# Optimization experiments

Measured on AMD Instinct MI355X. Metric: run time of the kernel, lower is better.

Reference implementation:

```python
import jax, jax.numpy as jnp
import numpy as np

B, N, C = 16, 256, 512
H, E = 8, 64
HD = C // H
SCALE = HD ** -0.5


def setup_inputs() -> dict:
    key = jax.random.key(0)
    ks = jax.random.split(key, 10)
    s = 0.02
    return {
        "node_embeds": jax.random.normal(ks[0], (B, N, C), jnp.float32),
        "edge_embeds": jax.random.normal(ks[1], (B, E, N, N), jnp.float32),
        "padding_mask": jnp.zeros((B, 1, N, N), bool),
        # params (torch Linear: y = x @ W.T + b, W is [out,in]; 1x1 Conv2d -> [out,in])
        "qkv_w": jax.random.normal(ks[2], (3 * C, C), jnp.float32) * s,
        "proj_w": jax.random.normal(ks[3], (C, C), jnp.float32) * s,
        "proj_b": jnp.zeros((C,), jnp.float32),
        "reduce_w": jax.random.normal(ks[4], (H, E), jnp.float32) * s,
        "reduce_b": jnp.zeros((H,), jnp.float32),
        "expand_w": jax.random.normal(ks[5], (E, H), jnp.float32) * s,
        "expand_b": jnp.zeros((E,), jnp.float32),
        "fc_w": jax.random.normal(ks[6], (C, E), jnp.float32) * s,
        "fc_b": jnp.zeros((C,), jnp.float32),
    }


def reference(node_embeds, edge_embeds, padding_mask, qkv_w, proj_w, proj_b,
              reduce_w, reduce_b, expand_w, expand_b, fc_w, fc_b):
    # qkv projection -> q,k,v each [B,H,N,HD]
    qkv = (node_embeds @ qkv_w.T).reshape(B, N, 3, H, HD)
    qkv = jnp.transpose(qkv, (2, 0, 3, 1, 4))
    q, k, v = qkv[0], qkv[1], qkv[2]

    attn = jnp.einsum("bhnd,bhmd->bhnm", q, k) * SCALE  # [B,H,N,N]
    # reduce: 1x1 conv over edge channels -> per-head bias
    attn_bias = jnp.einsum("bexy,he->bhxy", edge_embeds, reduce_w) + reduce_b[None, :, None, None]
    attn = attn + attn_bias
    residual = attn

    attn_sm = jax.nn.softmax(jnp.where(padding_mask, -jnp.inf, attn), axis=-1)
    node_out = jnp.einsum("bhnm,bhmd->bnhd", attn_sm, v).reshape(B, N, C)

    # expand: 1x1 conv heads -> edge channels on (attn_sm + residual)
    edge_out = jnp.einsum("bhxy,eh->bexy", attn_sm + residual, expand_w) + expand_b[None, :, None, None]

    # edge-update pooling: masked softmax over last dim, weighted sum
    w = jax.nn.softmax(jnp.where(padding_mask, -jnp.inf, edge_out), axis=-1)
    w = jnp.einsum("bexy->bxe", (w * edge_out).sum(-1)[:, :, :, None].squeeze(-1)[:, :, :, None].squeeze(-1)[..., None].squeeze(-1)[:, None].squeeze(1).reshape(B, E, N).transpose(0, 2, 1) * 1.0) if False else jnp.transpose((w * edge_out).sum(-1), (0, 2, 1))  # [B,N,E]

    node_out = node_out + (w @ fc_w.T + fc_b)
    node_out = node_out @ proj_w.T + proj_b
    return node_out, edge_out
```

## Files before the change

kernel.cpp:

```cpp
#include <hip/hip_runtime.h>
#include <hip/hip_bf16.h>
#include <cstdint>
#include <cstddef>

#define SCALE_ 0.125f

typedef float f4_ __attribute__((ext_vector_type(4)));
typedef __bf16 bf2_ __attribute__((ext_vector_type(2)));
typedef short bf8f_ __attribute__((ext_vector_type(8)));
typedef float f32x4_ __attribute__((ext_vector_type(4)));

__device__ __forceinline__ unsigned pk2(float a, float b) {
  union { __hip_bfloat16 h[2]; unsigned u; } x;
  x.h[0] = __float2bfloat16(a);
  x.h[1] = __float2bfloat16(b);
  return x.u;
}
__device__ __forceinline__ unsigned short bf16b(float a) {
  union { __hip_bfloat16 h; unsigned short s; } x;
  x.h = __float2bfloat16(a);
  return x.s;
}
__device__ __forceinline__ float blo(unsigned u) { return __uint_as_float(u << 16); }
__device__ __forceinline__ float bhi(unsigned u) { return __uint_as_float(u & 0xffff0000u); }
__device__ __forceinline__ float b2f(unsigned short s) { return __uint_as_float(((unsigned)s) << 16); }

__device__ __forceinline__ float dot2b(unsigned a, unsigned b, float c) {
#if __has_builtin(__builtin_amdgcn_fdot2_f32_bf16)
  return __builtin_amdgcn_fdot2_f32_bf16(__builtin_bit_cast(bf2_, a),
                                         __builtin_bit_cast(bf2_, b), c, false);
#else
  return fmaf(blo(a), blo(b), fmaf(bhi(a), bhi(b), c));
#endif
}

template<int CTRL, int RM>
__device__ __forceinline__ float dppadd(float v) {
  int x = __builtin_amdgcn_update_dpp(0, __float_as_int(v), CTRL, RM, 0xf, true);
  return v + __int_as_float(x);
}
__device__ __forceinline__ float wave_sum64(float v) {
  v = dppadd<0x111, 0xf>(v);
  v = dppadd<0x112, 0xf>(v);
  v = dppadd<0x114, 0xf>(v);
  v = dppadd<0x118, 0xf>(v);
  v = dppadd<0x142, 0xa>(v);
  v = dppadd<0x143, 0xc>(v);
  return __int_as_float(__builtin_amdgcn_readlane(__float_as_int(v), 63));
}

__global__ __launch_bounds__(256) void qkv_gemm(
    const float* __restrict__ X, const float* __restrict__ W,
    unsigned short* __restrict__ qb, uint2* __restrict__ ktq, uint2* __restrict__ vq)
{
  __shared__ alignas(16) unsigned ABbuf[128*36 + 64*36];
  unsigned* A_pk = ABbuf;
  unsigned* B_pk = ABbuf + 128*36;
  unsigned short* A16 = (unsigned short*)A_pk;
  unsigned short* B16 = (unsigned short*)B_pk;
  unsigned short* C16 = (unsigned short*)ABbuf;

  const int t  = threadIdx.x;
  const int lane = t & 63;
  const int wv = t >> 6;
  const int m0 = blockIdx.x * 128;
  const int o0 = blockIdx.y * 64;
  const int wrow = wv * 32;

  f32x4_ acc[2][4];
  #pragma unroll
  for (int fm = 0; fm < 2; fm++)
    #pragma unroll
    for (int fn = 0; fn < 4; fn++) acc[fm][fn] = (f32x4_){0.f, 0.f, 0.f, 0.f};

  const float4* X4 = (const float4*)X;
  const float4* W4 = (const float4*)W;

  for (int cc = 0; cc < 512; cc += 64) {
    #pragma unroll
    for (int i = 0; i < 8; i++) {
      int id = t + 256*i;
      int row = id >> 4, c4 = id & 15;
      float4 a = X4[(size_t)(m0 + row)*128 + (cc >> 2) + c4];
      A_pk[row*36 + c4*2    ] = pk2(a.x, a.y);
      A_pk[row*36 + c4*2 + 1] = pk2(a.z, a.w);
    }
    #pragma unroll
    for (int i = 0; i < 4; i++) {
      int id = t + 256*i;
      int row = id >> 4, c4 = id & 15;
      float4 w = W4[(size_t)(o0 + row)*128 + (cc >> 2) + c4];
      B_pk[row*36 + c4*2    ] = pk2(w.x, w.y);
      B_pk[row*36 + c4*2 + 1] = pk2(w.z, w.w);
    }
    __syncthreads();
    #pragma unroll
    for (int ks = 0; ks < 64; ks += 32) {
      const int kb = ks + (lane >> 4)*8;
      bf8f_ af0 = *(const bf8f_*)&A16[(wrow      + (lane & 15))*72 + kb];
      bf8f_ af1 = *(const bf8f_*)&A16[(wrow + 16 + (lane & 15))*72 + kb];
      #pragma unroll
      for (int fn = 0; fn < 4; fn++) {
        bf8f_ bf = *(const bf8f_*)&B16[(fn*16 + (lane & 15))*72 + kb];
        acc[0][fn] = __builtin_amdgcn_mfma_f32_16x16x32_bf16(af0, bf, acc[0][fn], 0, 0, 0);
        acc[1][fn] = __builtin_amdgcn_mfma_f32_16x16x32_bf16(af1, bf, acc[1][fn], 0, 0, 0);
      }
    }
    __syncthreads();
  }

  #pragma unroll
  for (int fm = 0; fm < 2; fm++)
    #pragma unroll
    for (int fn = 0; fn < 4; fn++)
      #pragma unroll
      for (int r = 0; r < 4; r++)
        C16[(wrow + fm*16 + (lane >> 4)*4 + r)*68 + fn*16 + (lane & 15)] =
          bf16b(acc[fm][fn][r]);
  __syncthreads();

  const int tm = (t & 15) * 8;
  const int to = (t >> 4) * 4;
  const int three = o0 >> 9;
  const int h = (o0 >> 6) & 7;
  if (three == 0) {
    #pragma unroll
    for (int i = 0; i < 8; i++) {
      int m = m0 + tm + i;
      int b = m >> 8, n = m & 255;
      uint2 u = *(const uint2*)&C16[(tm + i)*68 + to];
      *(uint2*)&qb[((size_t)(b*8 + h)*256 + n)*64 + to] = u;
    }
  } else if (three == 1) {
    #pragma unroll
    for (int i = 0; i < 8; i++) {
      int m = m0 + tm + i;
      int b = m >> 8, n = m & 255;
      uint2 u = *(const uint2*)&C16[(tm + i)*68 + to];
      ktq[(size_t)(b*8 + h)*4096 + (size_t)(to >> 2)*256 + n] = u;
    }
  } else {
    int m = m0 + tm;
    int b = m >> 8, n0 = m & 255;
    #pragma unroll
    for (int ii = 0; ii < 2; ii++) {
      #pragma unroll
      for (int j = 0; j < 4; j++) {
        unsigned ua = C16[(tm + 4*ii    )*68 + to + j];
        unsigned ub = C16[(tm + 4*ii + 1)*68 + to + j];
        unsigned uc = C16[(tm + 4*ii + 2)*68 + to + j];
        unsigned ud = C16[(tm + 4*ii + 3)*68 + to + j];
        vq[(size_t)(b*8 + h)*4096 + (size_t)((n0 >> 2) + ii)*64 + to + j] =
          make_uint2(ua | (ub << 16), uc | (ud << 16));
      }
    }
  }
}

__global__ __launch_bounds__(256) void fused_attn(
    const unsigned short* __restrict__ qb, const uint2* __restrict__ ktq,
    const uint2* __restrict__ vq,
    const float* __restrict__ edge, const unsigned char* __restrict__ mask,
    const float* __restrict__ rw, const float* __restrict__ rb,
    const float* __restrict__ ew, const float* __restrict__ eb,
    const float* __restrict__ fcw, const float* __restrict__ fcb,
    float* __restrict__ out_edge, unsigned short* __restrict__ tmpb)
{
  __shared__ alignas(16) unsigned q_pk[4][8][32];
  __shared__ alignas(16) unsigned char pt_raw[16896];
  __shared__ alignas(16) unsigned short nacc16[4][512];
  __shared__ alignas(16) unsigned rw_pk[32][8];
  __shared__ alignas(16) unsigned ew_pk[64][4];
  __shared__ alignas(16) float eb_s[64];
  __shared__ alignas(16) float pl2[4][64];
  __shared__ alignas(16) float inv_s[4][8];

  unsigned short (*p_sb)[8][264] = (unsigned short (*)[8][264])pt_raw;
  unsigned (*t8_pk)[4][264] = (unsigned (*)[4][264])pt_raw;

  const int t = threadIdx.x;
  const int lane = t & 63;
  const int wv = t >> 6;
  const int b = blockIdx.x >> 6;
  const int x0 = (blockIdx.x & 63) * 4;
  const int y = t;

  #pragma unroll
  for (int i = 0; i < 4; i++) {
    int id = t + i*256;
    int r = id >> 8, rest = id & 255;
    int h = rest >> 5, d2 = rest & 31;
    q_pk[r][h][d2] =
      *(const unsigned*)&qb[((size_t)(b*8 + h)*256 + x0 + r)*64 + d2*2];
  }
  { int epx = t >> 3, h = t & 7;
    rw_pk[epx][h] = pk2(rw[h*64 + 2*epx], rw[h*64 + 2*epx + 1]); }
  { int e = t >> 2, hp = t & 3;
    ew_pk[e][hp] = pk2(ew[(size_t)e*8 + 2*hp], ew[(size_t)e*8 + 2*hp + 1]); }
  if (t < 64) eb_s[t] = eb[t];
  float madd[4];
  #pragma unroll
  for (int r = 0; r < 4; r++)
    madd[r] = mask[(size_t)b*65536 + (size_t)(x0 + r)*256 + y] ? -1e30f : 0.f;
  __syncthreads();

  float acc[4][8];
  #pragma unroll
  for (int h = 0; h < 8; h++) {
    float rv = rb[h];
    #pragma unroll
    for (int r = 0; r < 4; r++) acc[r][h] = rv;
  }
  {
    const float* ep = edge + (size_t)b*(64*65536) + (size_t)x0*256 + y;
    #pragma unroll
    for (int h = 0; h < 8; h++) {
      const uint2* kq = ktq + (size_t)(b*8 + h)*4096 + y;
      float qk[4] = {0.f, 0.f, 0.f, 0.f};
      #pragma unroll
      for (int i = 0; i < 4; i++) {
        const int e2 = h*4 + i;
        unsigned vp[4];
        #pragma unroll
        for (int r = 0; r < 4; r++) {
          float a = __builtin_nontemporal_load(ep + (size_t)(2*e2)*65536 + r*256);
          float c = __builtin_nontemporal_load(ep + (size_t)(2*e2+1)*65536 + r*256);
          vp[r] = pk2(a, c);
        }
        uint4 w0 = *(const uint4*)&rw_pk[e2][0];
        uint4 w1 = *(const uint4*)&rw_pk[e2][4];
        unsigned wh[8] = {w0.x,w0.y,w0.z,w0.w,w1.x,w1.y,w1.z,w1.w};
        #pragma unroll
        for (int r = 0; r < 4; r++)
          #pragma unroll
          for (int hh = 0; hh < 8; hh++)
            acc[r][hh] = dot2b(vp[r], wh[hh], acc[r][hh]);
        #pragma unroll
        for (int dd = 0; dd < 4; dd++) {
          const int d4 = i*4 + dd;
          uint2 k = kq[(size_t)d4*256];
          #pragma unroll
          for (int r = 0; r < 4; r++) {
            uint2 qa = *(const uint2*)&q_pk[r][h][d4*2];
            qk[r] = dot2b(k.x, qa.x, qk[r]);
            qk[r] = dot2b(k.y, qa.y, qk[r]);
          }
        }
      }
      #pragma unroll
      for (int r = 0; r < 4; r++) acc[r][h] += SCALE_ * qk[r];
    }
  }

  #pragma unroll
  for (int r = 0; r < 4; r++)
    #pragma unroll
    for (int h = 0; h < 8; h++)
      p_sb[r][h][y] = bf16b(__expf(acc[r][h] + madd[r]));
  __syncthreads();

  {
    const int h = t >> 5;
    const int i2 = t & 31;
    const int d0 = i2 * 2;
    const unsigned ONES = 0x3F803F80u;
    const uint4* vp4 = (const uint4*)(vq + (size_t)(b*8 + h)*4096);
    float a[4][2], ps[4];
    #pragma unroll
    for (int r = 0; r < 4; r++) { a[r][0] = 0.f; a[r][1] = 0.f; ps[r] = 0.f; }
    #pragma unroll 2
    for (int y4 = 0; y4 < 64; y4++) {
      uint4 u = vp4[(size_t)y4*32 + i2];
      #pragma unroll
      for (int r = 0; r < 4; r++) {
        uint2 pp = *(const uint2*)&p_sb[r][h][y4*4];
        a[r][0] = dot2b(pp.x, u.x, a[r][0]); a[r][0] = dot2b(pp.y, u.y, a[r][0]);
        a[r][1] = dot2b(pp.x, u.z, a[r][1]); a[r][1] = dot2b(pp.y, u.w, a[r][1]);
        ps[r] = dot2b(pp.x, ONES, ps[r]);    ps[r] = dot2b(pp.y, ONES, ps[r]);
      }
    }
    #pragma unroll
    for (int r = 0; r < 4; r++) {
      float inv = 1.0f / ps[r];
      *(unsigned*)&nacc16[r][h*64 + d0] = pk2(a[r][0]*inv, a[r][1]*inv);
      if (i2 == 0) inv_s[r][h] = inv;
    }
  }
  __syncthreads();

  #pragma unroll
  for (int r = 0; r < 4; r++) {
    float v[8];
    #pragma unroll
    for (int h = 0; h < 8; h++)
      v[h] = __expf(acc[r][h] + madd[r]) * inv_s[r][h] + acc[r][h];
    t8_pk[r][0][y] = pk2(v[0], v[1]);
    t8_pk[r][1][y] = pk2(v[2], v[3]);
    t8_pk[r][2][y] = pk2(v[4], v[5]);
    t8_pk[r][3][y] = pk2(v[6], v[7]);
  }
  __syncthreads();

  {
    const int r = wv;
    const int y0 = lane * 4;
    const int xg = x0 + r;
    uint4 tfq[4];
    #pragma unroll
    for (int hp = 0; hp < 4; hp++) tfq[hp] = *(const uint4*)&t8_pk[r][hp][y0];
    uchar4 mb = *(const uchar4*)&mask[(size_t)b*65536 + (size_t)xg*256 + y0];
    const float md0 = mb.x ? -1e30f : 0.f;
    const float md1 = mb.y ? -1e30f : 0.f;
    const float md2 = mb.z ? -1e30f : 0.f;
    const float md3 = mb.w ? -1e30f : 0.f;
    for (int e = 0; e < 64; e++) {
      uint4 w = *(const uint4*)&ew_pk[e][0];
      float ebv = eb_s[e];
      float eo0 = dot2b(tfq[3].x, w.w, dot2b(tfq[2].x, w.z,
                  dot2b(tfq[1].x, w.y, dot2b(tfq[0].x, w.x, ebv))));
      float eo1 = dot2b(tfq[3].y, w.w, dot2b(tfq[2].y, w.z,
                  dot2b(tfq[1].y, w.y, dot2b(tfq[0].y, w.x, ebv))));
      float eo2 = dot2b(tfq[3].z, w.w, dot2b(tfq[2].z, w.z,
                  dot2b(tfq[1].z, w.y, dot2b(tfq[0].z, w.x, ebv))));
      float eo3 = dot2b(tfq[3].w, w.w, dot2b(tfq[2].w, w.z,
                  dot2b(tfq[1].w, w.y, dot2b(tfq[0].w, w.x, ebv))));
      float e0v = __expf(eo0+md0), e1v = __expf(eo1+md1);
      float e2v = __expf(eo2+md2), e3v = __expf(eo3+md3);
      float se  = (e0v + e1v) + (e2v + e3v);
      float swe = (e0v*eo0 + e1v*eo1) + (e2v*eo2 + e3v*eo3);
      se  = wave_sum64(se);
      swe = wave_sum64(swe);
      if (lane == 0) pl2[r][e] = swe / se;
      f4_ ov = {eo0, eo1, eo2, eo3};
      __builtin_nontemporal_store(ov,
        (f4_*)&out_edge[((size_t)(b*64 + e)*256 + xg)*256 + y0]);
    }
  }
  __syncthreads();

  #pragma unroll
  for (int pass = 0; pass < 2; pass++) {
    int cdx = t + pass*256;
    float bias_c = fcb[cdx];
    float a[4];
    #pragma unroll
    for (int r = 0; r < 4; r++) a[r] = b2f(nacc16[r][cdx]) + bias_c;
    const float4* fw4 = (const float4*)fcw;
    #pragma unroll 4
    for (int e4 = 0; e4 < 16; e4++) {
      float4 f = fw4[(size_t)cdx*16 + e4];
      #pragma unroll
      for (int r = 0; r < 4; r++) {
        float4 pl = *(const float4*)&pl2[r][e4*4];
        a[r] += pl.x*f.x + pl.y*f.y + pl.z*f.z + pl.w*f.w;
      }
    }
    #pragma unroll
    for (int r = 0; r < 4; r++)
      tmpb[((size_t)b*256 + x0 + r)*512 + cdx] = bf16b(a[r]);
  }
}

__global__ __launch_bounds__(256) void proj_gemm(
    const unsigned short* __restrict__ Xb, const float* __restrict__ W,
    const float* __restrict__ bias, float* __restrict__ out)
{
  __shared__ alignas(16) unsigned A_pk[8][132];
  __shared__ alignas(16) unsigned W_pk[8][68];
  const int t  = threadIdx.x;
  const int m0 = blockIdx.x * 128;
  const int o0 = blockIdx.y * 64;
  const int tm = (t & 15) * 8;
  const int to = (t >> 4) * 4;
  float acc[8][4];
  #pragma unroll
  for (int i = 0; i < 8; i++)
    #pragma unroll
    for (int j = 0; j < 4; j++) acc[i][j] = 0.f;

  const uint4* X4 = (const uint4*)Xb;
  const float4* W4 = (const float4*)W;
  for (int c0 = 0; c0 < 512; c0 += 16) {
    {
      int row = t >> 1, half = t & 1;
      uint4 a = X4[(size_t)(m0 + row) * 64 + (c0 >> 3) + half];
      A_pk[half*4 + 0][row] = a.x;
      A_pk[half*4 + 1][row] = a.y;
      A_pk[half*4 + 2][row] = a.z;
      A_pk[half*4 + 3][row] = a.w;
    }
    {
      int row = t >> 2, quad = t & 3;
      float4 w = W4[(size_t)(o0 + row) * 128 + (c0 >> 2) + quad];
      W_pk[quad*2    ][row] = pk2(w.x, w.y);
      W_pk[quad*2 + 1][row] = pk2(w.z, w.w);
    }
    __syncthreads();
    #pragma unroll
    for (int kp = 0; kp < 8; kp++) {
      uint4 a0 = *(const uint4*)&A_pk[kp][tm];
      uint4 a1 = *(const uint4*)&A_pk[kp][tm + 4];
      uint4 w0 = *(const uint4*)&W_pk[kp][to];
      unsigned am[8] = {a0.x,a0.y,a0.z,a0.w,a1.x,a1.y,a1.z,a1.w};
      unsigned wn[4] = {w0.x,w0.y,w0.z,w0.w};
      #pragma unroll
      for (int i = 0; i < 8; i++)
        #pragma unroll
        for (int j = 0; j < 4; j++) acc[i][j] = dot2b(am[i], wn[j], acc[i][j]);
    }
    __syncthreads();
  }
  float4 bb = *(const float4*)&bias[o0 + to];
  #pragma unroll
  for (int i = 0; i < 8; i++) {
    int m = m0 + tm + i;
    float4 r = make_float4(acc[i][0]+bb.x, acc[i][1]+bb.y, acc[i][2]+bb.z, acc[i][3]+bb.w);
    *(float4*)&out[(size_t)m*512 + o0 + to] = r;
  }
}

extern "C" void kernel_launch(void* const* d_in, const int* in_sizes, int n_in,
                              void* d_out, int out_size, void* d_ws, size_t ws_size,
                              hipStream_t stream)
{
  (void)in_sizes; (void)n_in; (void)out_size; (void)ws_size;
  const float* node   = (const float*)d_in[0];
  const float* edge   = (const float*)d_in[1];
  const unsigned char* mask = (const unsigned char*)d_in[2];
  const float* qkv_w  = (const float*)d_in[3];
  const float* proj_w = (const float*)d_in[4];
  const float* proj_b = (const float*)d_in[5];
  const float* rw     = (const float*)d_in[6];
  const float* rb     = (const float*)d_in[7];
  const float* ew     = (const float*)d_in[8];
  const float* eb     = (const float*)d_in[9];
  const float* fcw    = (const float*)d_in[10];
  const float* fcb    = (const float*)d_in[11];

  float* out_node = (float*)d_out;
  float* out_edge = out_node + (size_t)16*256*512;

  char* ws = (char*)d_ws;
  unsigned short* qb  = (unsigned short*)(ws);
  uint2*          ktq = (uint2*)         (ws + (size_t)4*1024*1024);
  uint2*          vq  = (uint2*)         (ws + (size_t)8*1024*1024);
  unsigned short* tmpb= (unsigned short*)(ws + (size_t)12*1024*1024);

  qkv_gemm <<<dim3(32, 24, 1), 256, 0, stream>>>(node, qkv_w, qb, ktq, vq);
  fused_attn<<<dim3(1024, 1, 1), 256, 0, stream>>>(qb, ktq, vq, edge, mask,
                                                   rw, rb, ew, eb, fcw, fcb,
                                                   out_edge, tmpb);
  proj_gemm<<<dim3(32, 8, 1), 256, 0, stream>>>(tmpb, proj_w, proj_b, out_node);
}
```

Before: 184.4 us.

## Use MFMA in projection GEMM and vectorize edge/key loads in fused attention

The projection GEMM drops its scalar dot2 bf16 loop in favour of MFMA 16x16x32 bf16 instructions, staging 64-wide K tiles in padded LDS. In the fused attention kernel, each thread now handles 2 rows x 2 adjacent columns instead of 4 rows x 1 column. This lets edge values load as float2 and K as uint4, and P is stored as packed bf16 pairs. The aim is fewer memory instructions and faster GEMM math, at the cost of changed LDS layouts and register use.

```diff
diff --git a/kernel.cpp b/kernel.cpp
--- a/kernel.cpp
+++ b/kernel.cpp
@@ -6,6 +6,7 @@
 #define SCALE_ 0.125f
 
 typedef float f4_ __attribute__((ext_vector_type(4)));
+typedef float f2_ __attribute__((ext_vector_type(2)));
 typedef __bf16 bf2_ __attribute__((ext_vector_type(2)));
 typedef short bf8f_ __attribute__((ext_vector_type(8)));
 typedef float f32x4_ __attribute__((ext_vector_type(4)));
@@ -175,7 +176,7 @@
   __shared__ alignas(16) float pl2[4][64];
   __shared__ alignas(16) float inv_s[4][8];
 
-  unsigned short (*p_sb)[8][264] = (unsigned short (*)[8][264])pt_raw;
+  unsigned (*p_pk)[8][132] = (unsigned (*)[8][132])pt_raw;
   unsigned (*t8_pk)[4][264] = (unsigned (*)[4][264])pt_raw;
 
   const int t = threadIdx.x;
@@ -183,7 +184,8 @@
   const int wv = t >> 6;
   const int b = blockIdx.x >> 6;
   const int x0 = (blockIdx.x & 63) * 4;
-  const int y = t;
+  const int yp = t & 127;
+  const int rg = t >> 7;
 
   #pragma unroll
   for (int i = 0; i < 4; i++) {
@@ -198,65 +200,80 @@
   { int e = t >> 2, hp = t & 3;
     ew_pk[e][hp] = pk2(ew[(size_t)e*8 + 2*hp], ew[(size_t)e*8 + 2*hp + 1]); }
   if (t < 64) eb_s[t] = eb[t];
-  float madd[4];
-  #pragma unroll
-  for (int r = 0; r < 4; r++)
-    madd[r] = mask[(size_t)b*65536 + (size_t)(x0 + r)*256 + y] ? -1e30f : 0.f;
-  __syncthreads();
-
-  float acc[4][8];
+  float madd[2][2];
+  #pragma unroll
+  for (int rr = 0; rr < 2; rr++) {
+    uchar2 mb = *(const uchar2*)&mask[(size_t)b*65536 + (size_t)(x0 + 2*rg + rr)*256 + 2*yp];
+    madd[rr][0] = mb.x ? -1e30f : 0.f;
+    madd[rr][1] = mb.y ? -1e30f : 0.f;
+  }
+  __syncthreads();
+
+  float acc[2][8][2];
   #pragma unroll
   for (int h = 0; h < 8; h++) {
     float rv = rb[h];
     #pragma unroll
-    for (int r = 0; r < 4; r++) acc[r][h] = rv;
+    for (int rr = 0; rr < 2; rr++) { acc[rr][h][0] = rv; acc[rr][h][1] = rv; }
   }
   {
-    const float* ep = edge + (size_t)b*(64*65536) + (size_t)x0*256 + y;
+    const float* ep = edge + (size_t)b*(64*65536) + (size_t)(x0 + 2*rg)*256 + 2*yp;
+    const uint4* kq4base = (const uint4*)(ktq + (size_t)(b*8)*4096);
     #pragma unroll
     for (int h = 0; h < 8; h++) {
-      const uint2* kq = ktq + (size_t)(b*8 + h)*4096 + y;
-      float qk[4] = {0.f, 0.f, 0.f, 0.f};
+      const uint4* kq4 = (const uint4*)(ktq + (size_t)(b*8 + h)*4096) ;
+      float qk[2][2] = {{0.f, 0.f}, {0.f, 0.f}};
       #pragma unroll
       for (int i = 0; i < 4; i++) {
         const int e2 = h*4 + i;
-        unsigned vp[4];
-        #pragma unroll
-        for (int r = 0; r < 4; r++) {
-          float a = __builtin_nontemporal_load(ep + (size_t)(2*e2)*65536 + r*256);
-          float c = __builtin_nontemporal_load(ep + (size_t)(2*e2+1)*65536 + r*256);
-          vp[r] = pk2(a, c);
-        }
+        f2_ A0 = __builtin_nontemporal_load((const f2_*)(ep + (size_t)(2*e2)*65536));
+        f2_ A1 = __builtin_nontemporal_load((const f2_*)(ep + (size_t)(2*e2)*65536 + 256));
+        f2_ B0 = __builtin_nontemporal_load((const f2_*)(ep + (size_t)(2*e2+1)*65536));
+        f2_ B1 = __builtin_nontemporal_load((const f2_*)(ep + (size_t)(2*e2+1)*65536 + 256));
+        unsigned vp00 = pk2(A0.x, B0.x);
+        unsigned vp01 = pk2(A0.y, B0.y);
+        unsigned vp10 = pk2(A1.x, B1.x);
+        unsigned vp11 = pk2(A1.y, B1.y);
         uint4 w0 = *(const uint4*)&rw_pk[e2][0];
         uint4 w1 = *(const uint4*)&rw_pk[e2][4];
         unsigned wh[8] = {w0.x,w0.y,w0.z,w0.w,w1.x,w1.y,w1.z,w1.w};
         #pragma unroll
-        for (int r = 0; r < 4; r++)
-          #pragma unroll
-          for (int hh = 0; hh < 8; hh++)
-            acc[r][hh] = dot2b(vp[r], wh[hh], acc[r][hh]);
+        for (int hh = 0; hh < 8; hh++) {
+          acc[0][hh][0] = dot2b(vp00, wh[hh], acc[0][hh][0]);
+          acc[0][hh][1] = dot2b(vp01, wh[hh], acc[0][hh][1]);
+          acc[1][hh][0] = dot2b(vp10, wh[hh], acc[1][hh][0]);
+          acc[1][hh][1] = dot2b(vp11, wh[hh], acc[1][hh][1]);
+        }
         #pragma unroll
         for (int dd = 0; dd < 4; dd++) {
           const int d4 = i*4 + dd;
-          uint2 k = kq[(size_t)d4*256];
+          uint4 kk = kq4[(size_t)d4*128 + yp];
           #pragma unroll
-          for (int r = 0; r < 4; r++) {
-            uint2 qa = *(const uint2*)&q_pk[r][h][d4*2];
-            qk[r] = dot2b(k.x, qa.x, qk[r]);
-            qk[r] = dot2b(k.y, qa.y, qk[r]);
+          for (int rr = 0; rr < 2; rr++) {
+            uint2 qa = *(const uint2*)&q_pk[2*rg + rr][h][d4*2];
+            qk[rr][0] = dot2b(kk.x, qa.x, qk[rr][0]);
+            qk[rr][0] = dot2b(kk.y, qa.y, qk[rr][0]);
+            qk[rr][1] = dot2b(kk.z, qa.x, qk[rr][1]);
+            qk[rr][1] = dot2b(kk.w, qa.y, qk[rr][1]);
           }
         }
       }
       #pragma unroll
-      for (int r = 0; r < 4; r++) acc[r][h] += SCALE_ * qk[r];
-    }
-  }
-
-  #pragma unroll
-  for (int r = 0; r < 4; r++)
+      for (int rr = 0; rr < 2; rr++) {
+        acc[rr][h][0] += SCALE_ * qk[rr][0];
+        acc[rr][h][1] += SCALE_ * qk[rr][1];
+      }
+    }
+    (void)kq4base;
+  }
+
+  #pragma unroll
+  for (int rr = 0; rr < 2; rr++)
     #pragma unroll
     for (int h = 0; h < 8; h++)
-      p_sb[r][h][y] = bf16b(__expf(acc[r][h] + madd[r]));
+      p_pk[2*rg + rr][h][yp] =
+        pk2(__expf(acc[rr][h][0] + madd[rr][0]),
+            __expf(acc[rr][h][1] + madd[rr][1]));
   __syncthreads();
 
   {
@@ -273,7 +290,7 @@
       uint4 u = vp4[(size_t)y4*32 + i2];
       #pragma unroll
       for (int r = 0; r < 4; r++) {
-        uint2 pp = *(const uint2*)&p_sb[r][h][y4*4];
+        uint2 pp = *(const uint2*)&p_pk[r][h][y4*2];
         a[r][0] = dot2b(pp.x, u.x, a[r][0]); a[r][0] = dot2b(pp.y, u.y, a[r][0]);
         a[r][1] = dot2b(pp.x, u.z, a[r][1]); a[r][1] = dot2b(pp.y, u.w, a[r][1]);
         ps[r] = dot2b(pp.x, ONES, ps[r]);    ps[r] = dot2b(pp.y, ONES, ps[r]);
@@ -289,15 +306,20 @@
   __syncthreads();
 
   #pragma unroll
-  for (int r = 0; r < 4; r++) {
-    float v[8];
-    #pragma unroll
-    for (int h = 0; h < 8; h++)
-      v[h] = __expf(acc[r][h] + madd[r]) * inv_s[r][h] + acc[r][h];
-    t8_pk[r][0][y] = pk2(v[0], v[1]);
-    t8_pk[r][1][y] = pk2(v[2], v[3]);
-    t8_pk[r][2][y] = pk2(v[4], v[5]);
-    t8_pk[r][3][y] = pk2(v[6], v[7]);
+  for (int rr = 0; rr < 2; rr++) {
+    const int r = 2*rg + rr;
+    #pragma unroll
+    for (int yy = 0; yy < 2; yy++) {
+      const int y = 2*yp + yy;
+      float v[8];
+      #pragma unroll
+      for (int h = 0; h < 8; h++)
+        v[h] = __expf(acc[rr][h][yy] + madd[rr][yy]) * inv_s[r][h] + acc[rr][h][yy];
+      t8_pk[r][0][y] = pk2(v[0], v[1]);
+      t8_pk[r][1][y] = pk2(v[2], v[3]);
+      t8_pk[r][2][y] = pk2(v[4], v[5]);
+      t8_pk[r][3][y] = pk2(v[6], v[7]);
+    }
   }
   __syncthreads();
 
@@ -365,57 +387,75 @@
     const unsigned short* __restrict__ Xb, const float* __restrict__ W,
     const float* __restrict__ bias, float* __restrict__ out)
 {
-  __shared__ alignas(16) unsigned A_pk[8][132];
-  __shared__ alignas(16) unsigned W_pk[8][68];
+  __shared__ alignas(16) unsigned ABbuf[128*36 + 64*36];
+  unsigned* A_pk = ABbuf;
+  unsigned* B_pk = ABbuf + 128*36;
+  unsigned short* A16 = (unsigned short*)A_pk;
+  unsigned short* B16 = (unsigned short*)B_pk;
+
   const int t  = threadIdx.x;
+  const int lane = t & 63;
+  const int wv = t >> 6;
   const int m0 = blockIdx.x * 128;
   const int o0 = blockIdx.y * 64;
-  const int tm = (t & 15) * 8;
-  const int to = (t >> 4) * 4;
-  float acc[8][4];
-  #pragma unroll
-  for (int i = 0; i < 8; i++)
-    #pragma unroll
-    for (int j = 0; j < 4; j++) acc[i][j] = 0.f;
+  const int wrow = wv * 32;
+
+  f32x4_ acc[2][4];
+  #pragma unroll
+  for (int fm = 0; fm < 2; fm++)
+    #pragma unroll
+    for (int fn = 0; fn < 4; fn++) acc[fm][fn] = (f32x4_){0.f, 0.f, 0.f, 0.f};
 
   const uint4* X4 = (const uint4*)Xb;
   const float4* W4 = (const float4*)W;
-  for (int c0 = 0; c0 < 512; c0 += 16) {
-    {
-      int row = t >> 1, half = t & 1;
-      uint4 a = X4[(size_t)(m0 + row) * 64 + (c0 >> 3) + half];
-      A_pk[half*4 + 0][row] = a.x;
-      A_pk[half*4 + 1][row] = a.y;
-      A_pk[half*4 + 2][row] = a.z;
-      A_pk[half*4 + 3][row] = a.w;
-    }
-    {
-      int row = t >> 2, quad = t & 3;
-      float4 w = W4[(size_t)(o0 + row) * 128 + (c0 >> 2) + quad];
-      W_pk[quad*2    ][row] = pk2(w.x, w.y);
-      W_pk[quad*2 + 1][row] = pk2(w.z, w.w);
+
+  for (int cc = 0; cc < 512; cc += 64) {
+    #pragma unroll
+    for (int i = 0; i < 4; i++) {
+      int id = t + 256*i;
+      int row = id >> 3, c8 = id & 7;
+      uint4 a = X4[(size_t)(m0 + row)*64 + (cc >> 3) + c8];
+      A_pk[row*36 + c8*4    ] = a.x;
+      A_pk[row*36 + c8*4 + 1] = a.y;
+      A_pk[row*36 + c8*4 + 2] = a.z;
+      A_pk[row*36 + c8*4 + 3] = a.w;
+    }
+    #pragma unroll
+    for (int i = 0; i < 4; i++) {
+      int id = t + 256*i;
+      int row = id >> 4, c4 = id & 15;
+      float4 w = W4[(size_t)(o0 + row)*128 + (cc >> 2) + c4];
+      B_pk[row*36 + c4*2    ] = pk2(w.x, w.y);
+      B_pk[row*36 + c4*2 + 1] = pk2(w.z, w.w);
     }
     __syncthreads();
     #pragma unroll
-    for (int kp = 0; kp < 8; kp++) {
-      uint4 a0 = *(const uint4*)&A_pk[kp][tm];
-      uint4 a1 = *(const uint4*)&A_pk[kp][tm + 4];
-      uint4 w0 = *(const uint4*)&W_pk[kp][to];
-      unsigned am[8] = {a0.x,a0.y,a0.z,a0.w,a1.x,a1.y,a1.z,a1.w};
-      unsigned wn[4] = {w0.x,w0.y,w0.z,w0.w};
-      #pragma unroll
-      for (int i = 0; i < 8; i++)
-        #pragma unroll
-        for (int j = 0; j < 4; j++) acc[i][j] = dot2b(am[i], wn[j], acc[i][j]);
+    for (int ks = 0; ks < 64; ks += 32) {
+      const int kb = ks + (lane >> 4)*8;
+      bf8f_ af0 = *(const bf8f_*)&A16[(wrow      + (lane & 15))*72 + kb];
+      bf8f_ af1 = *(const bf8f_*)&A16[(wrow + 16 + (lane & 15))*72 + kb];
+      #pragma unroll
+      for (int fn = 0; fn < 4; fn++) {
+        bf8f_ bf = *(const bf8f_*)&B16[(fn*16 + (lane & 15))*72 + kb];
+        acc[0][fn] = __builtin_amdgcn_mfma_f32_16x16x32_bf16(af0, bf, acc[0][fn], 0, 0, 0);
+        acc[1][fn] = __builtin_amdgcn_mfma_f32_16x16x32_bf16(af1, bf, acc[1][fn], 0, 0, 0);
+      }
     }
     __syncthreads();
   }
-  float4 bb = *(const float4*)&bias[o0 + to];
-  #pragma unroll
-  for (int i = 0; i < 8; i++) {
-    int m = m0 + tm + i;
-    float4 r = make_float4(acc[i][0]+bb.x, acc[i][1]+bb.y, acc[i][2]+bb.z, acc[i][3]+bb.w);
-    *(float4*)&out[(size_t)m*512 + o0 + to] = r;
+
+  #pragma unroll
+  for (int fn = 0; fn < 4; fn++) {
+    const int col = o0 + fn*16 + (lane & 15);
+    const float bb = bias[col];
+    #pragma unroll
+    for (int fm = 0; fm < 2; fm++) {
+      #pragma unroll
+      for (int r = 0; r < 4; r++) {
+        int m = m0 + wrow + fm*16 + (lane >> 4)*4 + r;
+        out[(size_t)m*512 + col] = acc[fm][fn][r] + bb;
+      }
+    }
   }
 }
 
```

Result: slower. 188.6 us (+2.3%).

## Rewrite output projection GEMM to use bf16 MFMA instructions

Applied to the files above, without the earlier changes.

The final projection GEMM moves from scalar bf16 dot2 accumulation to 16x16x32 bf16 MFMA matrix-core instructions. Each wave computes a 32x64 output tile. The shared-memory layout changes to row-major K-chunks of 64 with padded stride, and the K step grows from 16 to 64. The output stores become per-element scalar writes in the MFMA accumulator layout, which may be less coalesced than the previous float4 stores.

```diff
diff --git a/kernel.cpp b/kernel.cpp
--- a/kernel.cpp
+++ b/kernel.cpp
@@ -365,57 +365,75 @@
     const unsigned short* __restrict__ Xb, const float* __restrict__ W,
     const float* __restrict__ bias, float* __restrict__ out)
 {
-  __shared__ alignas(16) unsigned A_pk[8][132];
-  __shared__ alignas(16) unsigned W_pk[8][68];
+  __shared__ alignas(16) unsigned ABbuf[128*36 + 64*36];
+  unsigned* A_pk = ABbuf;
+  unsigned* B_pk = ABbuf + 128*36;
+  unsigned short* A16 = (unsigned short*)A_pk;
+  unsigned short* B16 = (unsigned short*)B_pk;
+
   const int t  = threadIdx.x;
+  const int lane = t & 63;
+  const int wv = t >> 6;
   const int m0 = blockIdx.x * 128;
   const int o0 = blockIdx.y * 64;
-  const int tm = (t & 15) * 8;
-  const int to = (t >> 4) * 4;
-  float acc[8][4];
-  #pragma unroll
-  for (int i = 0; i < 8; i++)
-    #pragma unroll
-    for (int j = 0; j < 4; j++) acc[i][j] = 0.f;
+  const int wrow = wv * 32;
+
+  f32x4_ acc[2][4];
+  #pragma unroll
+  for (int fm = 0; fm < 2; fm++)
+    #pragma unroll
+    for (int fn = 0; fn < 4; fn++) acc[fm][fn] = (f32x4_){0.f, 0.f, 0.f, 0.f};
 
   const uint4* X4 = (const uint4*)Xb;
   const float4* W4 = (const float4*)W;
-  for (int c0 = 0; c0 < 512; c0 += 16) {
-    {
-      int row = t >> 1, half = t & 1;
-      uint4 a = X4[(size_t)(m0 + row) * 64 + (c0 >> 3) + half];
-      A_pk[half*4 + 0][row] = a.x;
-      A_pk[half*4 + 1][row] = a.y;
-      A_pk[half*4 + 2][row] = a.z;
-      A_pk[half*4 + 3][row] = a.w;
-    }
-    {
-      int row = t >> 2, quad = t & 3;
-      float4 w = W4[(size_t)(o0 + row) * 128 + (c0 >> 2) + quad];
-      W_pk[quad*2    ][row] = pk2(w.x, w.y);
-      W_pk[quad*2 + 1][row] = pk2(w.z, w.w);
+
+  for (int cc = 0; cc < 512; cc += 64) {
+    #pragma unroll
+    for (int i = 0; i < 4; i++) {
+      int id = t + 256*i;
+      int row = id >> 3, c8 = id & 7;
+      uint4 a = X4[(size_t)(m0 + row)*64 + (cc >> 3) + c8];
+      A_pk[row*36 + c8*4    ] = a.x;
+      A_pk[row*36 + c8*4 + 1] = a.y;
+      A_pk[row*36 + c8*4 + 2] = a.z;
+      A_pk[row*36 + c8*4 + 3] = a.w;
+    }
+    #pragma unroll
+    for (int i = 0; i < 4; i++) {
+      int id = t + 256*i;
+      int row = id >> 4, c4 = id & 15;
+      float4 w = W4[(size_t)(o0 + row)*128 + (cc >> 2) + c4];
+      B_pk[row*36 + c4*2    ] = pk2(w.x, w.y);
+      B_pk[row*36 + c4*2 + 1] = pk2(w.z, w.w);
     }
     __syncthreads();
     #pragma unroll
-    for (int kp = 0; kp < 8; kp++) {
-      uint4 a0 = *(const uint4*)&A_pk[kp][tm];
-      uint4 a1 = *(const uint4*)&A_pk[kp][tm + 4];
-      uint4 w0 = *(const uint4*)&W_pk[kp][to];
-      unsigned am[8] = {a0.x,a0.y,a0.z,a0.w,a1.x,a1.y,a1.z,a1.w};
-      unsigned wn[4] = {w0.x,w0.y,w0.z,w0.w};
-      #pragma unroll
-      for (int i = 0; i < 8; i++)
-        #pragma unroll
-        for (int j = 0; j < 4; j++) acc[i][j] = dot2b(am[i], wn[j], acc[i][j]);
+    for (int ks = 0; ks < 64; ks += 32) {
+      const int kb = ks + (lane >> 4)*8;
+      bf8f_ af0 = *(const bf8f_*)&A16[(wrow      + (lane & 15))*72 + kb];
+      bf8f_ af1 = *(const bf8f_*)&A16[(wrow + 16 + (lane & 15))*72 + kb];
+      #pragma unroll
+      for (int fn = 0; fn < 4; fn++) {
+        bf8f_ bf = *(const bf8f_*)&B16[(fn*16 + (lane & 15))*72 + kb];
+        acc[0][fn] = __builtin_amdgcn_mfma_f32_16x16x32_bf16(af0, bf, acc[0][fn], 0, 0, 0);
+        acc[1][fn] = __builtin_amdgcn_mfma_f32_16x16x32_bf16(af1, bf, acc[1][fn], 0, 0, 0);
+      }
     }
     __syncthreads();
   }
-  float4 bb = *(const float4*)&bias[o0 + to];
-  #pragma unroll
-  for (int i = 0; i < 8; i++) {
-    int m = m0 + tm + i;
-    float4 r = make_float4(acc[i][0]+bb.x, acc[i][1]+bb.y, acc[i][2]+bb.z, acc[i][3]+bb.w);
-    *(float4*)&out[(size_t)m*512 + o0 + to] = r;
+
+  #pragma unroll
+  for (int fn = 0; fn < 4; fn++) {
+    const int col = o0 + fn*16 + (lane & 15);
+    const float bb = bias[col];
+    #pragma unroll
+    for (int fm = 0; fm < 2; fm++) {
+      #pragma unroll
+      for (int r = 0; r < 4; r++) {
+        int m = m0 + wrow + fm*16 + (lane >> 4)*4 + r;
+        out[(size_t)m*512 + col] = acc[fm][fn][r] + bb;
+      }
+    }
   }
 }
 
```

After: 162.3 us (median of 2 runs). 12.0% less time.
